# Kernel optimization log

Measured on AMD Instinct MI355X. Metric: run time of the kernel, lower is better.

The kernel has to match this reference:

```python
import jax, jax.numpy as jnp
import numpy as np


def setup_inputs() -> dict:
    key = jax.random.key(0)
    ks = jax.random.split(key, 8)
    B, T, C = 4, 1024, 1024
    s = 1.0 / np.sqrt(C)
    return {
        "q": jax.random.normal(ks[0], (B, T, C), jnp.float32),
        "k": jax.random.normal(ks[1], (B, T, C), jnp.float32),
        "v": jax.random.normal(ks[2], (B, T, C), jnp.float32),
        "Wq": jax.random.normal(ks[3], (C, C), jnp.float32) * s,
        "Wk": jax.random.normal(ks[4], (C, C), jnp.float32) * s,
        "Wv": jax.random.normal(ks[5], (C, C), jnp.float32) * s,
        "Wp": jax.random.normal(ks[6], (C, C), jnp.float32) * s,
        "bp": jnp.zeros((C,), jnp.float32),
        "n_head": 16,
        "kernel_size": 16,
    }


def reference(q, k, v, Wq, Wk, Wv, Wp, bp, n_head, kernel_size):
    B, T, C = q.shape
    H = n_head
    D = C // H

    def split_heads(x, W):
        # nn.Linear applies x @ W.T
        return (x @ W.T).reshape(B, T, H, D).transpose(0, 2, 1, 3)  # (B,H,T,D)

    qp = split_heads(q, Wq)
    kp = split_heads(k, Wk)
    vp = split_heads(v, Wv)

    # Faithful to the torch double loop: wei[b,h,i,j] = sum over feature dims
    # d in [max(0, j-ks), min(T, j+ks)) (clipped to [0,D)) of qp[b,h,i,d]*kp[b,h,i,d] / sqrt(D).
    # Both windows index sequence position i; the window slides over the head_dim axis.
    p = qp * kp / jnp.sqrt(jnp.asarray(D, qp.dtype))          # (B,H,T,D)
    cs = jnp.cumsum(p, axis=-1)
    cs = jnp.concatenate([jnp.zeros(cs.shape[:-1] + (1,), cs.dtype), cs], axis=-1)  # (B,H,T,D+1)
    j = jnp.arange(T)
    start = jnp.clip(j - kernel_size, 0, D)                   # (T,)
    end = jnp.clip(jnp.minimum(j + kernel_size, T), 0, D)     # (T,)
    wei = cs[..., end] - cs[..., start]                       # (B,H,T,T): windowed partial dot of row i

    attn = jax.nn.softmax(wei, axis=-1)
    out = jnp.einsum("bhts,bhsd->bhtd", attn, vp)             # (B,H,T,D)
    out = out.transpose(0, 2, 1, 3).reshape(B, T, C)
    out = out @ Wp.T + bp
    # dropout is identity in eval mode
    return out
```

## Files before the change

### kernel.cpp

```cpp
#include <hip/hip_runtime.h>
#include <hip/hip_bf16.h>
#include <stdint.h>


typedef __bf16 bf16x8 __attribute__((ext_vector_type(8)));
typedef float f32x4 __attribute__((ext_vector_type(4)));

#define AS1(p) ((__attribute__((address_space(1))) void*)(p))
#define AS3(p) ((__attribute__((address_space(3))) void*)(p))

__global__ __launch_bounds__(256) void cvt_kernel(
    const float* __restrict__ q, const float* __restrict__ k,
    const float* __restrict__ v, const float* __restrict__ Wq,
    const float* __restrict__ Wk, const float* __restrict__ Wv,
    const float* __restrict__ Wp,
    ushort4* __restrict__ qkv_bf, ushort4* __restrict__ w_bf)
{
  int idx = blockIdx.x * 256 + threadIdx.x;
  const float* src; ushort4* dst; int i;
  if (idx < 3145728) {
    int which = idx >> 20; i = idx & 1048575;
    src = which == 0 ? q : which == 1 ? k : v;
    dst = qkv_bf + (size_t)which * 1048576 + i;
  } else {
    int w = idx - 3145728; int which = w >> 18; i = w & 262143;
    src = which == 0 ? Wq : which == 1 ? Wk : which == 2 ? Wv : Wp;
    dst = w_bf + w;
  }
  float4 val = ((const float4*)src)[i];
  union { ushort4 u; __hip_bfloat16 h[4]; } c;
  c.h[0] = __float2bfloat16(val.x); c.h[1] = __float2bfloat16(val.y);
  c.h[2] = __float2bfloat16(val.z); c.h[3] = __float2bfloat16(val.w);
  dst[0] = c.u;
}

template <typename OutT>
__device__ __forceinline__ void gemm_tile128(
    const __hip_bfloat16* __restrict__ A, const __hip_bfloat16* __restrict__ Bw,
    OutT* __restrict__ C, const float* __restrict__ bias)
{
  const int N = 1024, K = 1024;
  __shared__ __align__(16) __hip_bfloat16 As[2][128 * 32];
  __shared__ __align__(16) __hip_bfloat16 Bs[2][128 * 32];
  const int t = threadIdx.x;
  const int wv = t >> 6, lane = t & 63;
  const int wRow = (wv >> 1) * 64, wCol = (wv & 1) * 64;
  const int mrow = lane & 15, kq = lane >> 4;

  f32x4 acc[4][4] = {};

  for (int k0 = 0; k0 < K; k0 += 64) {
    __syncthreads();
#pragma unroll
    for (int half = 0; half < 2; ++half)
#pragma unroll
      for (int tI = 0; tI < 2; ++tI) {
        int chunk = wv * 2 + tI;
        int byteOff = chunk * 1024 + lane * 16;
        int row = byteOff >> 6;
        int colEl = (byteOff & 63) >> 1;
        const __hip_bfloat16* ga = A + (size_t)row * K + k0 + half * 32 + colEl;
        __builtin_amdgcn_global_load_lds(AS1((void*)ga), AS3(&As[half][chunk * 512]), 16, 0, 0);
        const __hip_bfloat16* gb = Bw + (size_t)row * K + k0 + half * 32 + colEl;
        __builtin_amdgcn_global_load_lds(AS1((void*)gb), AS3(&Bs[half][chunk * 512]), 16, 0, 0);
      }
    __syncthreads();

#pragma unroll
    for (int half = 0; half < 2; ++half) {
      bf16x8 af[4], bf[4];
#pragma unroll
      for (int mi = 0; mi < 4; ++mi)
        af[mi] = *(const bf16x8*)&As[half][(wRow + mi * 16 + mrow) * 32 + kq * 8];
#pragma unroll
      for (int ni = 0; ni < 4; ++ni)
        bf[ni] = *(const bf16x8*)&Bs[half][(wCol + ni * 16 + mrow) * 32 + kq * 8];
#pragma unroll
      for (int mi = 0; mi < 4; ++mi)
#pragma unroll
        for (int ni = 0; ni < 4; ++ni)
          acc[mi][ni] = __builtin_amdgcn_mfma_f32_16x16x32_bf16(af[mi], bf[ni], acc[mi][ni], 0, 0, 0);
    }
  }

#pragma unroll
  for (int mi = 0; mi < 4; ++mi)
#pragma unroll
    for (int ni = 0; ni < 4; ++ni)
#pragma unroll
      for (int r = 0; r < 4; ++r) {
        int row = wRow + mi * 16 + kq * 4 + r;
        int col = wCol + ni * 16 + mrow;
        float val = acc[mi][ni][r];
        if (bias) val += bias[col];
        if constexpr (__is_same(OutT, __hip_bfloat16))
          C[(size_t)row * N + col] = __float2bfloat16(val);
        else
          C[(size_t)row * N + col] = val;
      }
}

__global__ __launch_bounds__(256) void qkv_gemm_kernel(
    const __hip_bfloat16* __restrict__ QKVbf, const __hip_bfloat16* __restrict__ Wbf,
    __hip_bfloat16* __restrict__ QKVp)
{
  int l = blockIdx.x;
  int n = l / 96, mm = l % 96, z = mm >> 5, m = mm & 31;
  gemm_tile128<__hip_bfloat16>(
      QKVbf + (size_t)z * 4194304 + (size_t)m * 131072,
      Wbf + (size_t)z * 1048576 + (size_t)n * 131072,
      QKVp + (size_t)z * 4194304 + (size_t)m * 131072 + n * 128, nullptr);
}

__global__ __launch_bounds__(256) void final_gemm_kernel(
    const __hip_bfloat16* __restrict__ Abf, const __hip_bfloat16* __restrict__ Wpbf,
    float* __restrict__ Out, const float* __restrict__ biasAll)
{
  const int N = 1024, K = 1024;
  int l = blockIdx.x;
  int m = l & 63, n = l >> 6;
  const __hip_bfloat16* A = Abf + (size_t)m * 65536;
  const __hip_bfloat16* Bw = Wpbf + (size_t)n * 131072;
  float* C = Out + (size_t)m * 65536 + n * 128;
  const float* bias = biasAll + n * 128;

  __shared__ __align__(16) __hip_bfloat16 As[2][64 * 32];
  __shared__ __align__(16) __hip_bfloat16 Bs[2][128 * 32];
  const int t = threadIdx.x;
  const int wv = t >> 6, lane = t & 63;
  const int wRow = (wv >> 1) * 32, wCol = (wv & 1) * 64;
  const int mrow = lane & 15, kq = lane >> 4;

  f32x4 acc[2][4] = {};

  for (int k0 = 0; k0 < K; k0 += 64) {
    __syncthreads();
#pragma unroll
    for (int tI = 0; tI < 6; ++tI) {
      int c = wv * 6 + tI;
      int byteOff, row, colEl;
      if (c < 8) {
        int half = c >> 2, ch = c & 3;
        byteOff = ch * 1024 + lane * 16;
        row = byteOff >> 6; colEl = (byteOff & 63) >> 1;
        const __hip_bfloat16* ga = A + (size_t)row * K + k0 + half * 32 + colEl;
        __builtin_amdgcn_global_load_lds(AS1((void*)ga), AS3(&As[half][ch * 512]), 16, 0, 0);
      } else {
        int cb = c - 8, half = cb >> 3, ch = cb & 7;
        byteOff = ch * 1024 + lane * 16;
        row = byteOff >> 6; colEl = (byteOff & 63) >> 1;
        const __hip_bfloat16* gb = Bw + (size_t)row * K + k0 + half * 32 + colEl;
        __builtin_amdgcn_global_load_lds(AS1((void*)gb), AS3(&Bs[half][ch * 512]), 16, 0, 0);
      }
    }
    __syncthreads();

#pragma unroll
    for (int half = 0; half < 2; ++half) {
      bf16x8 af[2], bf[4];
#pragma unroll
      for (int mi = 0; mi < 2; ++mi)
        af[mi] = *(const bf16x8*)&As[half][(wRow + mi * 16 + mrow) * 32 + kq * 8];
#pragma unroll
      for (int ni = 0; ni < 4; ++ni)
        bf[ni] = *(const bf16x8*)&Bs[half][(wCol + ni * 16 + mrow) * 32 + kq * 8];
#pragma unroll
      for (int mi = 0; mi < 2; ++mi)
#pragma unroll
        for (int ni = 0; ni < 4; ++ni)
          acc[mi][ni] = __builtin_amdgcn_mfma_f32_16x16x32_bf16(af[mi], bf[ni], acc[mi][ni], 0, 0, 0);
    }
  }

#pragma unroll
  for (int mi = 0; mi < 2; ++mi)
#pragma unroll
    for (int ni = 0; ni < 4; ++ni)
#pragma unroll
      for (int r = 0; r < 4; ++r) {
        int row = wRow + mi * 16 + kq * 4 + r;
        int col = wCol + ni * 16 + mrow;
        C[(size_t)row * N + col] = acc[mi][ni][r] + bias[col];
      }
}

__global__ __launch_bounds__(256) void tail_partial_kernel(
    const __hip_bfloat16* __restrict__ VP, float* __restrict__ partial)
{
  const int seg = blockIdx.x, bh = blockIdx.y;
  const int b = bh >> 4, h = bh & 15;
  const int d = threadIdx.x & 63, wv = threadIdx.x >> 6;
  const int jBase = 80 + seg * 59;
  float s = 0.0f;
  for (int r = wv; r < 59; r += 4)
    s += __bfloat162float(VP[((size_t)(b * 1024 + jBase + r)) * 1024 + h * 64 + d]);
  __shared__ float red[4][64];
  red[wv][d] = s;
  __syncthreads();
  if (threadIdx.x < 64)
    partial[(bh * 16 + seg) * 64 + threadIdx.x] =
        red[0][threadIdx.x] + red[1][threadIdx.x] + red[2][threadIdx.x] + red[3][threadIdx.x];
}

__global__ __launch_bounds__(256) void attn_kernel(
    const __hip_bfloat16* __restrict__ QP, const __hip_bfloat16* __restrict__ KP,
    const __hip_bfloat16* __restrict__ VP, const float* __restrict__ partial,
    __hip_bfloat16* __restrict__ OUTA)
{
  const int b = blockIdx.z, h = blockIdx.y, i0 = blockIdx.x * 64;
  const int t = threadIdx.x, lane = t & 63, wv = t >> 6;

  __shared__ __align__(16) char bufA[64 * 68 * 4];
  float (*csl)[68] = (float(*)[68])bufA;
  __hip_bfloat16 (*vpt)[104] = (__hip_bfloat16(*)[104])bufA;
  __shared__ __align__(16) __hip_bfloat16 wlb[64][96];
  __shared__ float scl[64], tlw[64], tail[64];

  if (t < 64) {
    const float* pp = partial + (b * 16 + h) * 16 * 64 + t;
    float s = 0.0f;
#pragma unroll
    for (int seg = 0; seg < 16; ++seg) s += pp[seg * 64];
    tail[t] = s;
  }

  {
    const int i = t >> 2, seg = t & 3;
    const size_t base = ((size_t)(b * 1024 + i0 + i)) * 1024 + h * 64 + seg * 16;
    bf16x8 q0 = *(const bf16x8*)(QP + base);
    bf16x8 q1 = *(const bf16x8*)(QP + base + 8);
    bf16x8 k0 = *(const bf16x8*)(KP + base);
    bf16x8 k1 = *(const bf16x8*)(KP + base + 8);
    float cs[16];
    float run = 0.0f;
#pragma unroll
    for (int x = 0; x < 8; ++x) {
      run += (float)q0[x] * (float)k0[x] * 0.125f;
      cs[x] = run;
    }
#pragma unroll
    for (int x = 0; x < 8; ++x) {
      run += (float)q1[x] * (float)k1[x] * 0.125f;
      cs[8 + x] = run;
    }
    float t1 = __shfl_up(run, 1, 4);
    float t2 = __shfl_up(run, 2, 4);
    float t3 = __shfl_up(run, 3, 4);
    float off = 0.0f;
    if (seg > 0) off += t1;
    if (seg > 1) off += t2;
    if (seg > 2) off += t3;
    float4* dst = (float4*)&csl[i][seg * 16];
#pragma unroll
    for (int x4 = 0; x4 < 4; ++x4)
      dst[x4] = make_float4(cs[4 * x4] + off, cs[4 * x4 + 1] + off,
                            cs[4 * x4 + 2] + off, cs[4 * x4 + 3] + off);
  }
  __syncthreads();

  {
    int i = t >> 2, jg = t & 3;
    float wloc[20];
    float mx = 0.0f;
#pragma unroll
    for (int q = 0; q < 20; ++q) {
      int j = jg + 4 * q;
      int s = j - 16; s = s < 0 ? 0 : s;
      int e = j + 16; e = e > 64 ? 64 : e;
      float w = csl[i][e - 1] - (s > 0 ? csl[i][s - 1] : 0.0f);
      wloc[q] = w;
      mx = fmaxf(mx, w);
    }
    mx = fmaxf(mx, __shfl_xor(mx, 1, 64));
    mx = fmaxf(mx, __shfl_xor(mx, 2, 64));
    float sum = 0.0f;
#pragma unroll
    for (int q = 0; q < 20; ++q) {
      float e_ = __expf(wloc[q] - mx);
      wlb[i][jg + 4 * q] = __float2bfloat16(e_);
      sum += e_;
    }
#pragma unroll
    for (int q = 0; q < 4; ++q)
      wlb[i][80 + jg + 4 * q] = __float2bfloat16(0.0f);
    sum += __shfl_xor(sum, 1, 64);
    sum += __shfl_xor(sum, 2, 64);
    float tw = __expf(-mx);
    sum += 944.0f * tw;
    if (jg == 0) { scl[i] = 1.0f / sum; tlw[i] = tw / sum; }
  }
  __syncthreads();

  for (int idx = t; idx < 80 * 64; idx += 256) {
    int j = idx >> 6, d = idx & 63;
    vpt[d][j] = VP[((size_t)(b * 1024 + j)) * 1024 + h * 64 + d];
  }
  for (int idx = t; idx < 64 * 16; idx += 256) {
    int d = idx >> 4, j = 80 + (idx & 15);
    vpt[d][j] = __float2bfloat16(0.0f);
  }
  __syncthreads();

  {
    const int mh = (wv >> 1) * 32, nh = (wv & 1) * 32;
    const int mrow = lane & 15, kq = lane >> 4;
    f32x4 acc[2][2] = {};
#pragma unroll
    for (int k0 = 0; k0 < 96; k0 += 32) {
      bf16x8 af[2], bf[2];
#pragma unroll
      for (int mi = 0; mi < 2; ++mi)
        af[mi] = *(const bf16x8*)&wlb[mh + mi * 16 + mrow][k0 + kq * 8];
#pragma unroll
      for (int ni = 0; ni < 2; ++ni)
        bf[ni] = *(const bf16x8*)&vpt[nh + ni * 16 + mrow][k0 + kq * 8];
#pragma unroll
      for (int mi = 0; mi < 2; ++mi)
#pragma unroll
        for (int ni = 0; ni < 2; ++ni)
          acc[mi][ni] = __builtin_amdgcn_mfma_f32_16x16x32_bf16(af[mi], bf[ni], acc[mi][ni], 0, 0, 0);
    }
#pragma unroll
    for (int mi = 0; mi < 2; ++mi)
#pragma unroll
      for (int ni = 0; ni < 2; ++ni)
#pragma unroll
        for (int r = 0; r < 4; ++r) {
          int i = mh + mi * 16 + kq * 4 + r;
          int d = nh + ni * 16 + mrow;
          float o = acc[mi][ni][r] * scl[i] + tlw[i] * tail[d];
          OUTA[((size_t)(b * 1024 + i0 + i)) * 1024 + h * 64 + d] = __float2bfloat16(o);
        }
  }
}

extern "C" void kernel_launch(void* const* d_in, const int* in_sizes, int n_in,
                              void* d_out, int out_size, void* d_ws, size_t ws_size,
                              hipStream_t stream)
{
  (void)in_sizes; (void)n_in; (void)out_size; (void)ws_size;
  const float* q  = (const float*)d_in[0];
  const float* k  = (const float*)d_in[1];
  const float* v  = (const float*)d_in[2];
  const float* Wq = (const float*)d_in[3];
  const float* Wk = (const float*)d_in[4];
  const float* Wv = (const float*)d_in[5];
  const float* Wp = (const float*)d_in[6];
  const float* bp = (const float*)d_in[7];

  char* ws = (char*)d_ws;
  __hip_bfloat16* qkv_bf = (__hip_bfloat16*)(ws);
  __hip_bfloat16* w_bf   = (__hip_bfloat16*)(ws + 25165824);
  __hip_bfloat16* QKVp   = (__hip_bfloat16*)(ws + 33554432);
  __hip_bfloat16* OUTA   = (__hip_bfloat16*)(ws + 58720256);
  float* partial = (float*)(ws);
  float* out = (float*)d_out;

  cvt_kernel<<<dim3(16384), 256, 0, stream>>>(q, k, v, Wq, Wk, Wv, Wp,
      (ushort4*)qkv_bf, (ushort4*)w_bf);
  qkv_gemm_kernel<<<dim3(768), 256, 0, stream>>>(qkv_bf, w_bf, QKVp);
  tail_partial_kernel<<<dim3(16, 64), 256, 0, stream>>>(QKVp + (size_t)2 * 4194304, partial);
  attn_kernel<<<dim3(16, 16, 4), 256, 0, stream>>>(QKVp, QKVp + (size_t)4194304,
                                                   QKVp + (size_t)2 * 4194304, partial, OUTA);
  final_gemm_kernel<<<dim3(512), 256, 0, stream>>>(OUTA, w_bf + (size_t)3 * 1048576,
                                                   out, bp);
}
```

Measured before the change: 182.3 us.

## Fuse V tail-sum into QKV GEMM epilogue; shrink final GEMM tile

The per-column sum of V rows at index 80 and above is now accumulated in the QKV GEMM epilogue through wave shuffles and atomicAdd into a zeroed buffer. This removes the separate tail_partial kernel launch and its re-read of V. The final projection GEMM moves from 64x128 to 64x64 tiles, doubling the block count to 1024 for better CU occupancy. The cost is a memset, atomic contention, fp32 accumulation order that is not deterministic, and less data reuse in the final GEMM.

```diff
diff --git a/kernel.cpp b/kernel.cpp
--- a/kernel.cpp
+++ b/kernel.cpp
@@ -34,10 +34,9 @@
   dst[0] = c.u;
 }
 
-template <typename OutT>
 __device__ __forceinline__ void gemm_tile128(
     const __hip_bfloat16* __restrict__ A, const __hip_bfloat16* __restrict__ Bw,
-    OutT* __restrict__ C, const float* __restrict__ bias)
+    __hip_bfloat16* __restrict__ C, float* tailAtomic, int rowInB)
 {
   const int N = 1024, K = 1024;
   __shared__ __align__(16) __hip_bfloat16 As[2][128 * 32];
@@ -91,25 +90,41 @@
       for (int r = 0; r < 4; ++r) {
         int row = wRow + mi * 16 + kq * 4 + r;
         int col = wCol + ni * 16 + mrow;
-        float val = acc[mi][ni][r];
-        if (bias) val += bias[col];
-        if constexpr (__is_same(OutT, __hip_bfloat16))
-          C[(size_t)row * N + col] = __float2bfloat16(val);
-        else
-          C[(size_t)row * N + col] = val;
+        C[(size_t)row * N + col] = __float2bfloat16(acc[mi][ni][r]);
       }
+
+  if (tailAtomic) {
+#pragma unroll
+    for (int ni = 0; ni < 4; ++ni) {
+      float s = 0.0f;
+#pragma unroll
+      for (int mi = 0; mi < 4; ++mi)
+#pragma unroll
+        for (int r = 0; r < 4; ++r) {
+          int localRow = rowInB + wRow + mi * 16 + kq * 4 + r;
+          if (localRow >= 80) s += acc[mi][ni][r];
+        }
+      s += __shfl_xor(s, 16, 64);
+      s += __shfl_xor(s, 32, 64);
+      if (kq == 0) atomicAdd(&tailAtomic[wCol + ni * 16 + mrow], s);
+    }
+  }
 }
 
 __global__ __launch_bounds__(256) void qkv_gemm_kernel(
     const __hip_bfloat16* __restrict__ QKVbf, const __hip_bfloat16* __restrict__ Wbf,
-    __hip_bfloat16* __restrict__ QKVp)
+    __hip_bfloat16* __restrict__ QKVp, float* __restrict__ tails)
 {
   int l = blockIdx.x;
   int n = l / 96, mm = l % 96, z = mm >> 5, m = mm & 31;
-  gemm_tile128<__hip_bfloat16>(
+  float* tailAtomic = nullptr;
+  int rowInB = (m & 7) * 128;
+  if (z == 2) tailAtomic = tails + (size_t)(m >> 3) * 1024 + n * 128;
+  gemm_tile128(
       QKVbf + (size_t)z * 4194304 + (size_t)m * 131072,
       Wbf + (size_t)z * 1048576 + (size_t)n * 131072,
-      QKVp + (size_t)z * 4194304 + (size_t)m * 131072 + n * 128, nullptr);
+      QKVp + (size_t)z * 4194304 + (size_t)m * 131072 + n * 128,
+      tailAtomic, rowInB);
 }
 
 __global__ __launch_bounds__(256) void final_gemm_kernel(
@@ -120,54 +135,53 @@
   int l = blockIdx.x;
   int m = l & 63, n = l >> 6;
   const __hip_bfloat16* A = Abf + (size_t)m * 65536;
-  const __hip_bfloat16* Bw = Wpbf + (size_t)n * 131072;
-  float* C = Out + (size_t)m * 65536 + n * 128;
-  const float* bias = biasAll + n * 128;
+  const __hip_bfloat16* Bw = Wpbf + (size_t)n * 65536;
+  float* C = Out + (size_t)m * 65536 + n * 64;
+  const float* bias = biasAll + n * 64;
 
   __shared__ __align__(16) __hip_bfloat16 As[2][64 * 32];
-  __shared__ __align__(16) __hip_bfloat16 Bs[2][128 * 32];
+  __shared__ __align__(16) __hip_bfloat16 Bs[2][64 * 32];
   const int t = threadIdx.x;
   const int wv = t >> 6, lane = t & 63;
-  const int wRow = (wv >> 1) * 32, wCol = (wv & 1) * 64;
+  const int wRow = (wv >> 1) * 32, wCol = (wv & 1) * 32;
   const int mrow = lane & 15, kq = lane >> 4;
 
-  f32x4 acc[2][4] = {};
+  f32x4 acc[2][2] = {};
 
   for (int k0 = 0; k0 < K; k0 += 64) {
     __syncthreads();
 #pragma unroll
-    for (int tI = 0; tI < 6; ++tI) {
-      int c = wv * 6 + tI;
-      int byteOff, row, colEl;
-      if (c < 8) {
-        int half = c >> 2, ch = c & 3;
-        byteOff = ch * 1024 + lane * 16;
-        row = byteOff >> 6; colEl = (byteOff & 63) >> 1;
-        const __hip_bfloat16* ga = A + (size_t)row * K + k0 + half * 32 + colEl;
-        __builtin_amdgcn_global_load_lds(AS1((void*)ga), AS3(&As[half][ch * 512]), 16, 0, 0);
-      } else {
-        int cb = c - 8, half = cb >> 3, ch = cb & 7;
-        byteOff = ch * 1024 + lane * 16;
-        row = byteOff >> 6; colEl = (byteOff & 63) >> 1;
-        const __hip_bfloat16* gb = Bw + (size_t)row * K + k0 + half * 32 + colEl;
-        __builtin_amdgcn_global_load_lds(AS1((void*)gb), AS3(&Bs[half][ch * 512]), 16, 0, 0);
+    for (int tI = 0; tI < 4; ++tI) {
+      int c = wv * 4 + tI;
+      int half, ch;
+      const __hip_bfloat16* gsrc;
+      __hip_bfloat16* ldst;
+      if (c < 8) { half = c >> 2; ch = c & 3;
+        int byteOff = ch * 1024 + lane * 16;
+        gsrc = A + (size_t)(byteOff >> 6) * K + k0 + half * 32 + ((byteOff & 63) >> 1);
+        ldst = &As[half][ch * 512];
+      } else { int cb = c - 8; half = cb >> 2; ch = cb & 3;
+        int byteOff = ch * 1024 + lane * 16;
+        gsrc = Bw + (size_t)(byteOff >> 6) * K + k0 + half * 32 + ((byteOff & 63) >> 1);
+        ldst = &Bs[half][ch * 512];
       }
+      __builtin_amdgcn_global_load_lds(AS1((void*)gsrc), AS3(ldst), 16, 0, 0);
     }
     __syncthreads();
 
 #pragma unroll
     for (int half = 0; half < 2; ++half) {
-      bf16x8 af[2], bf[4];
+      bf16x8 af[2], bf[2];
 #pragma unroll
       for (int mi = 0; mi < 2; ++mi)
         af[mi] = *(const bf16x8*)&As[half][(wRow + mi * 16 + mrow) * 32 + kq * 8];
 #pragma unroll
-      for (int ni = 0; ni < 4; ++ni)
+      for (int ni = 0; ni < 2; ++ni)
         bf[ni] = *(const bf16x8*)&Bs[half][(wCol + ni * 16 + mrow) * 32 + kq * 8];
 #pragma unroll
       for (int mi = 0; mi < 2; ++mi)
 #pragma unroll
-        for (int ni = 0; ni < 4; ++ni)
+        for (int ni = 0; ni < 2; ++ni)
           acc[mi][ni] = __builtin_amdgcn_mfma_f32_16x16x32_bf16(af[mi], bf[ni], acc[mi][ni], 0, 0, 0);
     }
   }
@@ -175,7 +189,7 @@
 #pragma unroll
   for (int mi = 0; mi < 2; ++mi)
 #pragma unroll
-    for (int ni = 0; ni < 4; ++ni)
+    for (int ni = 0; ni < 2; ++ni)
 #pragma unroll
       for (int r = 0; r < 4; ++r) {
         int row = wRow + mi * 16 + kq * 4 + r;
@@ -184,27 +198,9 @@
       }
 }
 
-__global__ __launch_bounds__(256) void tail_partial_kernel(
-    const __hip_bfloat16* __restrict__ VP, float* __restrict__ partial)
-{
-  const int seg = blockIdx.x, bh = blockIdx.y;
-  const int b = bh >> 4, h = bh & 15;
-  const int d = threadIdx.x & 63, wv = threadIdx.x >> 6;
-  const int jBase = 80 + seg * 59;
-  float s = 0.0f;
-  for (int r = wv; r < 59; r += 4)
-    s += __bfloat162float(VP[((size_t)(b * 1024 + jBase + r)) * 1024 + h * 64 + d]);
-  __shared__ float red[4][64];
-  red[wv][d] = s;
-  __syncthreads();
-  if (threadIdx.x < 64)
-    partial[(bh * 16 + seg) * 64 + threadIdx.x] =
-        red[0][threadIdx.x] + red[1][threadIdx.x] + red[2][threadIdx.x] + red[3][threadIdx.x];
-}
-
 __global__ __launch_bounds__(256) void attn_kernel(
     const __hip_bfloat16* __restrict__ QP, const __hip_bfloat16* __restrict__ KP,
-    const __hip_bfloat16* __restrict__ VP, const float* __restrict__ partial,
+    const __hip_bfloat16* __restrict__ VP, const float* __restrict__ tails,
     __hip_bfloat16* __restrict__ OUTA)
 {
   const int b = blockIdx.z, h = blockIdx.y, i0 = blockIdx.x * 64;
@@ -216,13 +212,7 @@
   __shared__ __align__(16) __hip_bfloat16 wlb[64][96];
   __shared__ float scl[64], tlw[64], tail[64];
 
-  if (t < 64) {
-    const float* pp = partial + (b * 16 + h) * 16 * 64 + t;
-    float s = 0.0f;
-#pragma unroll
-    for (int seg = 0; seg < 16; ++seg) s += pp[seg * 64];
-    tail[t] = s;
-  }
+  if (t < 64) tail[t] = tails[(size_t)b * 1024 + h * 64 + t];
 
   {
     const int i = t >> 2, seg = t & 3;
@@ -353,15 +343,15 @@
   __hip_bfloat16* w_bf   = (__hip_bfloat16*)(ws + 25165824);
   __hip_bfloat16* QKVp   = (__hip_bfloat16*)(ws + 33554432);
   __hip_bfloat16* OUTA   = (__hip_bfloat16*)(ws + 58720256);
-  float* partial = (float*)(ws);
+  float*          tails  = (float*)(ws + 67108864);
   float* out = (float*)d_out;
 
+  hipMemsetAsync(tails, 0, 4096 * sizeof(float), stream);
   cvt_kernel<<<dim3(16384), 256, 0, stream>>>(q, k, v, Wq, Wk, Wv, Wp,
       (ushort4*)qkv_bf, (ushort4*)w_bf);
-  qkv_gemm_kernel<<<dim3(768), 256, 0, stream>>>(qkv_bf, w_bf, QKVp);
-  tail_partial_kernel<<<dim3(16, 64), 256, 0, stream>>>(QKVp + (size_t)2 * 4194304, partial);
+  qkv_gemm_kernel<<<dim3(768), 256, 0, stream>>>(qkv_bf, w_bf, QKVp, tails);
   attn_kernel<<<dim3(16, 16, 4), 256, 0, stream>>>(QKVp, QKVp + (size_t)4194304,
-                                                   QKVp + (size_t)2 * 4194304, partial, OUTA);
-  final_gemm_kernel<<<dim3(512), 256, 0, stream>>>(OUTA, w_bf + (size_t)3 * 1048576,
-                                                   out, bp);
-}
+                                                   QKVp + (size_t)2 * 4194304, tails, OUTA);
+  final_gemm_kernel<<<dim3(1024), 256, 0, stream>>>(OUTA, w_bf + (size_t)3 * 1048576,
+                                                    out, bp);
+}
```

Result: faster. 177.9 us (-2.4%).
